# Kernel optimization log

Hardware: AMD Instinct MI355X
Metric: run time of the kernel (lower is better)

## Reference

```python
import jax, jax.numpy as jnp
import numpy as np

MARGIN = 1.0
EPS = 1e-12  # safe sqrt/normalize clamp; used entries have magnitude >> EPS


def _normalize(x):
    return x / jnp.maximum(jnp.linalg.norm(x, axis=-1, keepdims=True), EPS)


def _cdist(x, y):
    # Pairwise L2 distances, matches torch.cdist(p=2)
    sq = (jnp.sum(x * x, axis=-1)[:, None]
          + jnp.sum(y * y, axis=-1)[None, :]
          - 2.0 * (x @ y.T))
    return jnp.sqrt(jnp.maximum(sq, EPS))


def setup_inputs() -> dict:
    key = jax.random.key(0)
    k1, k2, k3 = jax.random.split(key, 3)
    B, P, D = 4096, 2, 256
    anchor = jax.random.normal(k1, (B, D), dtype=jnp.float32)
    positive = jax.random.normal(k2, (B, P, D), dtype=jnp.float32)
    labels = jax.random.randint(k3, (B,), 0, 200)
    return {"anchor": anchor, "positive": positive, "labels": labels}


def reference(anchor, positive, labels):
    a = _normalize(anchor)            # [B, D]
    p = _normalize(positive)          # [B, P, D]
    B = a.shape[0]
    all_labels = jnp.concatenate([labels, labels])           # [2B]
    neg_mask = all_labels[None, :] != labels[:, None]        # [B, 2B]
    idx = jnp.arange(B)
    losses = []
    for v in range(p.shape[1]):  # loop over small fixed num_positives
        feats = jnp.concatenate([a, p[:, v]], axis=0)        # [2B, D]
        dist = _cdist(feats, feats)                          # [2B, 2B]
        pos_dist = dist[idx, idx + B]                        # [B]
        # hard negative mining: min distance over different-label columns
        neg_dist = jnp.min(jnp.where(neg_mask, dist[:B], jnp.inf), axis=1)  # [B]
        losses.append(jnp.maximum(pos_dist - neg_dist + MARGIN, 0.0))
    return jnp.mean(jnp.stack(losses))
```

## Files before the change

### kernel.cpp

```cpp
#include <hip/hip_runtime.h>
#include <hip/hip_bf16.h>

#define NB    4096
#define ND    256
#define NP    2
#define TOT   (NB * 3)
#define NCHUNK 24
#define COLS_PER_CHUNK (TOT / NCHUNK)
#define TILES (COLS_PER_CHUNK / 16)
#define PITCH 528
#define NEG_INIT (-4.0f)

typedef __bf16 bf16x8 __attribute__((ext_vector_type(8)));
typedef float  f32x4  __attribute__((ext_vector_type(4)));

#define WS_F_OFF    0
#define WS_POS_OFF  (TOT * ND * 2)
#define WS_PART_OFF (WS_POS_OFF + NB * NP * 4)

__device__ __forceinline__ unsigned short f2bf(float f) {
    unsigned u = __float_as_uint(f);
    u += 0x7fffu + ((u >> 16) & 1u);
    return (unsigned short)(u >> 16);
}

__global__ void norm_pos_kernel(const float* __restrict__ anchor,
                                const float* __restrict__ positive,
                                unsigned short* __restrict__ F,
                                float* __restrict__ posArr) {
    int wid = threadIdx.x >> 6, lane = threadIdx.x & 63;
    int row = blockIdx.x * 4 + wid;
    if (row < NB) {
        const float* src = anchor + (size_t)row * ND;
        float4 x = *(const float4*)(src + lane * 4);
        float ss = x.x * x.x + x.y * x.y + x.z * x.z + x.w * x.w;
        #pragma unroll
        for (int m = 1; m < 64; m <<= 1) ss += __shfl_xor(ss, m, 64);
        float inv = 1.0f / fmaxf(sqrtf(ss), 1e-12f);
        ushort4 o;
        o.x = f2bf(x.x * inv); o.y = f2bf(x.y * inv);
        o.z = f2bf(x.z * inv); o.w = f2bf(x.w * inv);
        *(ushort4*)(F + (size_t)row * ND + lane * 4) = o;
    } else {
        int q = row - NB;
        int v = q >> 12;
        int j = q & (NB - 1);
        const float* sp = positive + (size_t)(j * NP + v) * ND;
        const float* sa = anchor + (size_t)j * ND;
        float4 xp = *(const float4*)(sp + lane * 4);
        float4 xa = *(const float4*)(sa + lane * 4);
        float sspv = xp.x * xp.x + xp.y * xp.y + xp.z * xp.z + xp.w * xp.w;
        float ssa  = xa.x * xa.x + xa.y * xa.y + xa.z * xa.z + xa.w * xa.w;
        float dot  = xa.x * xp.x + xa.y * xp.y + xa.z * xp.z + xa.w * xp.w;
        #pragma unroll
        for (int m = 1; m < 64; m <<= 1) {
            sspv += __shfl_xor(sspv, m, 64);
            ssa  += __shfl_xor(ssa, m, 64);
            dot  += __shfl_xor(dot, m, 64);
        }
        float invp = 1.0f / fmaxf(sqrtf(sspv), 1e-12f);
        ushort4 o;
        o.x = f2bf(xp.x * invp); o.y = f2bf(xp.y * invp);
        o.z = f2bf(xp.z * invp); o.w = f2bf(xp.w * invp);
        *(ushort4*)(F + (size_t)row * ND + lane * 4) = o;
        if (lane == 0) {
            float inva = 1.0f / fmaxf(sqrtf(ssa), 1e-12f);
            float dn = dot * inva * invp;
            float sq = 2.0f - 2.0f * dn;
            posArr[j * NP + v] = sqrtf(fmaxf(sq, 1e-12f));
        }
    }
}

__global__ __launch_bounds__(256) void gram_max_kernel(
        const unsigned short* __restrict__ F,
        const int* __restrict__ labels,
        float* __restrict__ partials) {
    __shared__ unsigned char lds[2][16 * PITCH];
    int tid = threadIdx.x;
    int wid = tid >> 6, lane = tid & 63;
    int l15 = lane & 15, quad = lane >> 4;
    int rowBase = blockIdx.x * 128 + wid * 32;
    int chunk = blockIdx.y;
    int col0 = chunk * COLS_PER_CHUNK;
    int part = col0 >> 12;
    const unsigned char* Fb = (const unsigned char*)F;

    int scol = tid >> 4, sseg = tid & 15;

    bf16x8 af[2][8];
    #pragma unroll
    for (int s = 0; s < 2; ++s) {
        const unsigned char* ar = Fb + (size_t)(rowBase + s * 16 + l15) * 512 + quad * 16;
        #pragma unroll
        for (int kk = 0; kk < 8; ++kk)
            af[s][kk] = *(const bf16x8*)(ar + kk * 64);
    }
    int rl[2][4];
    #pragma unroll
    for (int s = 0; s < 2; ++s)
        #pragma unroll
        for (int r = 0; r < 4; ++r)
            rl[s][r] = labels[rowBase + s * 16 + quad * 4 + r];

    float vmax[2][4];
    #pragma unroll
    for (int s = 0; s < 2; ++s)
        #pragma unroll
        for (int r = 0; r < 4; ++r) vmax[s][r] = NEG_INIT;

    float4 r0, r1;
    auto gload = [&](int ct) {
        const unsigned char* g = Fb + (size_t)(col0 + ct * 16 + scol) * 512 + sseg * 16;
        r0 = *(const float4*)g;
        r1 = *(const float4*)(g + 256);
    };
    auto swrite = [&](int buf) {
        unsigned char* p = &lds[buf][scol * PITCH + sseg * 16];
        *(float4*)p = r0;
        *(float4*)(p + 256) = r1;
    };

    gload(0); swrite(0);
    gload(1);
    __syncthreads();

    for (int ct = 0; ct < TILES; ++ct) {
        int buf = ct & 1;
        bf16x8 bfr[8];
        #pragma unroll
        for (int kk = 0; kk < 8; ++kk)
            bfr[kk] = *(const bf16x8*)&lds[buf][l15 * PITCH + quad * 16 + kk * 64];

        if (ct + 1 < TILES) swrite(buf ^ 1);
        if (ct + 2 < TILES) gload(ct + 2);

        int c = col0 + ct * 16 + l15;
        int lc = labels[c & (NB - 1)];

        f32x4 acc0a = {0.f,0.f,0.f,0.f}, acc0b = {0.f,0.f,0.f,0.f};
        f32x4 acc1a = {0.f,0.f,0.f,0.f}, acc1b = {0.f,0.f,0.f,0.f};
        #pragma unroll
        for (int kk = 0; kk < 4; ++kk) {
            acc0a = __builtin_amdgcn_mfma_f32_16x16x32_bf16(af[0][kk],   bfr[kk],   acc0a, 0, 0, 0);
            acc0b = __builtin_amdgcn_mfma_f32_16x16x32_bf16(af[0][kk+4], bfr[kk+4], acc0b, 0, 0, 0);
            acc1a = __builtin_amdgcn_mfma_f32_16x16x32_bf16(af[1][kk],   bfr[kk],   acc1a, 0, 0, 0);
            acc1b = __builtin_amdgcn_mfma_f32_16x16x32_bf16(af[1][kk+4], bfr[kk+4], acc1b, 0, 0, 0);
        }
        #pragma unroll
        for (int r = 0; r < 4; ++r) {
            float d0 = acc0a[r] + acc0b[r], d1 = acc1a[r] + acc1b[r];
            vmax[0][r] = fmaxf(vmax[0][r], (lc != rl[0][r]) ? d0 : NEG_INIT);
            vmax[1][r] = fmaxf(vmax[1][r], (lc != rl[1][r]) ? d1 : NEG_INIT);
        }
        __syncthreads();
    }

    #pragma unroll
    for (int m = 1; m < 16; m <<= 1)
        #pragma unroll
        for (int s = 0; s < 2; ++s)
            #pragma unroll
            for (int r = 0; r < 4; ++r)
                vmax[s][r] = fmaxf(vmax[s][r], __shfl_xor(vmax[s][r], m, 64));

    if (l15 == 0) {
        #pragma unroll
        for (int s = 0; s < 2; ++s)
            #pragma unroll
            for (int r = 0; r < 4; ++r) {
                int row = rowBase + s * 16 + quad * 4 + r;
                partials[(size_t)part * NB * 8 + (size_t)row * 8 + (chunk & 7)] = vmax[s][r];
            }
    }
}

__global__ void finalize_kernel(const float* __restrict__ partials,
                                const float* __restrict__ posArr,
                                float* __restrict__ out) {
    int row = blockIdx.x * 256 + threadIdx.x;
    const float* pa = partials + (size_t)row * 8;
    const float* pb = pa + (size_t)NB * 8;
    const float* pc = pb + (size_t)NB * 8;
    float ma = NEG_INIT, m0 = NEG_INIT, m1 = NEG_INIT;
    #pragma unroll
    for (int j = 0; j < 8; ++j) {
        ma = fmaxf(ma, pa[j]);
        m0 = fmaxf(m0, pb[j]);
        m1 = fmaxf(m1, pc[j]);
    }
    float n0 = sqrtf(fmaxf(2.0f - 2.0f * fmaxf(ma, m0), 1e-12f));
    float n1 = sqrtf(fmaxf(2.0f - 2.0f * fmaxf(ma, m1), 1e-12f));
    float l = fmaxf(posArr[row * 2 + 0] - n0 + 1.0f, 0.0f)
            + fmaxf(posArr[row * 2 + 1] - n1 + 1.0f, 0.0f);
    int lane = threadIdx.x & 63, wid = threadIdx.x >> 6;
    #pragma unroll
    for (int m = 1; m < 64; m <<= 1) l += __shfl_xor(l, m, 64);
    __shared__ float wsum[4];
    if (lane == 0) wsum[wid] = l;
    __syncthreads();
    if (threadIdx.x == 0) {
        float s = wsum[0] + wsum[1] + wsum[2] + wsum[3];
        atomicAdd(out, s * (1.0f / (NB * NP)));
    }
}

extern "C" void kernel_launch(void* const* d_in, const int* in_sizes, int n_in,
                              void* d_out, int out_size, void* d_ws, size_t ws_size,
                              hipStream_t stream) {
    const float* anchor   = (const float*)d_in[0];
    const float* positive = (const float*)d_in[1];
    const int*   labels   = (const int*)d_in[2];
    float* out = (float*)d_out;

    unsigned short* F = (unsigned short*)((char*)d_ws + WS_F_OFF);
    float* posArr     = (float*)((char*)d_ws + WS_POS_OFF);
    float* partials   = (float*)((char*)d_ws + WS_PART_OFF);

    norm_pos_kernel<<<TOT / 4, 256, 0, stream>>>(anchor, positive, F, posArr);
    gram_max_kernel<<<dim3(NB / 128, NCHUNK), 256, 0, stream>>>(F, labels, partials);
    hipMemsetAsync(d_out, 0, sizeof(float), stream);
    finalize_kernel<<<NB / 256, 256, 0, stream>>>(partials, posArr, out);
}
```

Before: 102.7 us.

## Give each wave 64 rows, halve block size, stage column labels in LDS

The Gram/max kernel now runs 2 waves per block, each holding 64 A rows (4 MFMA row tiles) instead of 32, so every B tile loaded from LDS feeds twice as many MFMAs. Column labels are preloaded into shared memory once per block, and row labels are packed as bytes so four label comparisons become one XOR. The aim is to raise MFMA work per LDS read and cut per-tile label loads, at the cost of more registers per thread and fewer waves per block, which may lower occupancy and latency hiding. Byte packing assumes labels are below 256.

```diff
diff --git a/kernel.cpp b/kernel.cpp
--- a/kernel.cpp
+++ b/kernel.cpp
@@ -72,53 +72,57 @@
     }
 }
 
-__global__ __launch_bounds__(256) void gram_max_kernel(
+__global__ __launch_bounds__(128) void gram_max_kernel(
         const unsigned short* __restrict__ F,
         const int* __restrict__ labels,
         float* __restrict__ partials) {
     __shared__ unsigned char lds[2][16 * PITCH];
+    __shared__ int slab[COLS_PER_CHUNK];
     int tid = threadIdx.x;
     int wid = tid >> 6, lane = tid & 63;
     int l15 = lane & 15, quad = lane >> 4;
-    int rowBase = blockIdx.x * 128 + wid * 32;
+    int rowBase = blockIdx.x * 128 + wid * 64;
     int chunk = blockIdx.y;
     int col0 = chunk * COLS_PER_CHUNK;
     int part = col0 >> 12;
     const unsigned char* Fb = (const unsigned char*)F;
 
-    int scol = tid >> 4, sseg = tid & 15;
-
-    bf16x8 af[2][8];
-    #pragma unroll
-    for (int s = 0; s < 2; ++s) {
+    ((int4*)slab)[tid] = ((const int4*)(labels + (col0 & (NB - 1))))[tid];
+
+    int scol = tid >> 3, sseg = tid & 7;
+
+    bf16x8 af[4][8];
+    #pragma unroll
+    for (int s = 0; s < 4; ++s) {
         const unsigned char* ar = Fb + (size_t)(rowBase + s * 16 + l15) * 512 + quad * 16;
         #pragma unroll
         for (int kk = 0; kk < 8; ++kk)
             af[s][kk] = *(const bf16x8*)(ar + kk * 64);
     }
-    int rl[2][4];
-    #pragma unroll
-    for (int s = 0; s < 2; ++s)
-        #pragma unroll
-        for (int r = 0; r < 4; ++r)
-            rl[s][r] = labels[rowBase + s * 16 + quad * 4 + r];
-
-    float vmax[2][4];
-    #pragma unroll
-    for (int s = 0; s < 2; ++s)
+    unsigned rlp[4];
+    #pragma unroll
+    for (int s = 0; s < 4; ++s) {
+        const int* lb = labels + rowBase + s * 16 + quad * 4;
+        rlp[s] = (unsigned)lb[0] | ((unsigned)lb[1] << 8)
+               | ((unsigned)lb[2] << 16) | ((unsigned)lb[3] << 24);
+    }
+
+    float vmax[4][4];
+    #pragma unroll
+    for (int s = 0; s < 4; ++s)
         #pragma unroll
         for (int r = 0; r < 4; ++r) vmax[s][r] = NEG_INIT;
 
-    float4 r0, r1;
+    float4 rg[4];
     auto gload = [&](int ct) {
-        const unsigned char* g = Fb + (size_t)(col0 + ct * 16 + scol) * 512 + sseg * 16;
-        r0 = *(const float4*)g;
-        r1 = *(const float4*)(g + 256);
+        const unsigned char* g = Fb + (size_t)(col0 + ct * 16 + scol) * 512 + sseg * 64;
+        #pragma unroll
+        for (int j = 0; j < 4; ++j) rg[j] = *(const float4*)(g + j * 16);
     };
     auto swrite = [&](int buf) {
-        unsigned char* p = &lds[buf][scol * PITCH + sseg * 16];
-        *(float4*)p = r0;
-        *(float4*)(p + 256) = r1;
+        unsigned char* p = &lds[buf][scol * PITCH + sseg * 64];
+        #pragma unroll
+        for (int j = 0; j < 4; ++j) *(float4*)(p + j * 16) = rg[j];
     };
 
     gload(0); swrite(0);
@@ -135,23 +139,26 @@
         if (ct + 1 < TILES) swrite(buf ^ 1);
         if (ct + 2 < TILES) gload(ct + 2);
 
-        int c = col0 + ct * 16 + l15;
-        int lc = labels[c & (NB - 1)];
-
-        f32x4 acc0a = {0.f,0.f,0.f,0.f}, acc0b = {0.f,0.f,0.f,0.f};
-        f32x4 acc1a = {0.f,0.f,0.f,0.f}, acc1b = {0.f,0.f,0.f,0.f};
-        #pragma unroll
-        for (int kk = 0; kk < 4; ++kk) {
-            acc0a = __builtin_amdgcn_mfma_f32_16x16x32_bf16(af[0][kk],   bfr[kk],   acc0a, 0, 0, 0);
-            acc0b = __builtin_amdgcn_mfma_f32_16x16x32_bf16(af[0][kk+4], bfr[kk+4], acc0b, 0, 0, 0);
-            acc1a = __builtin_amdgcn_mfma_f32_16x16x32_bf16(af[1][kk],   bfr[kk],   acc1a, 0, 0, 0);
-            acc1b = __builtin_amdgcn_mfma_f32_16x16x32_bf16(af[1][kk+4], bfr[kk+4], acc1b, 0, 0, 0);
-        }
-        #pragma unroll
-        for (int r = 0; r < 4; ++r) {
-            float d0 = acc0a[r] + acc0b[r], d1 = acc1a[r] + acc1b[r];
-            vmax[0][r] = fmaxf(vmax[0][r], (lc != rl[0][r]) ? d0 : NEG_INIT);
-            vmax[1][r] = fmaxf(vmax[1][r], (lc != rl[1][r]) ? d1 : NEG_INIT);
+        int lc = slab[ct * 16 + l15];
+        unsigned lcq = (unsigned)lc * 0x01010101u;
+
+        f32x4 acc[4];
+        #pragma unroll
+        for (int s = 0; s < 4; ++s) acc[s] = (f32x4){0.f, 0.f, 0.f, 0.f};
+        #pragma unroll
+        for (int kk = 0; kk < 8; ++kk)
+            #pragma unroll
+            for (int s = 0; s < 4; ++s)
+                acc[s] = __builtin_amdgcn_mfma_f32_16x16x32_bf16(af[s][kk], bfr[kk], acc[s], 0, 0, 0);
+
+        #pragma unroll
+        for (int s = 0; s < 4; ++s) {
+            unsigned x = rlp[s] ^ lcq;
+            #pragma unroll
+            for (int r = 0; r < 4; ++r) {
+                bool neq = ((x >> (8 * r)) & 0xffu) != 0u;
+                vmax[s][r] = fmaxf(vmax[s][r], neq ? acc[s][r] : NEG_INIT);
+            }
         }
         __syncthreads();
     }
@@ -159,14 +166,14 @@
     #pragma unroll
     for (int m = 1; m < 16; m <<= 1)
         #pragma unroll
-        for (int s = 0; s < 2; ++s)
+        for (int s = 0; s < 4; ++s)
             #pragma unroll
             for (int r = 0; r < 4; ++r)
                 vmax[s][r] = fmaxf(vmax[s][r], __shfl_xor(vmax[s][r], m, 64));
 
     if (l15 == 0) {
         #pragma unroll
-        for (int s = 0; s < 2; ++s)
+        for (int s = 0; s < 4; ++s)
             #pragma unroll
             for (int r = 0; r < 4; ++r) {
                 int row = rowBase + s * 16 + quad * 4 + r;
@@ -218,7 +225,7 @@
     float* partials   = (float*)((char*)d_ws + WS_PART_OFF);
 
     norm_pos_kernel<<<TOT / 4, 256, 0, stream>>>(anchor, positive, F, posArr);
-    gram_max_kernel<<<dim3(NB / 128, NCHUNK), 256, 0, stream>>>(F, labels, partials);
+    gram_max_kernel<<<dim3(NB / 128, NCHUNK), 128, 0, stream>>>(F, labels, partials);
     hipMemsetAsync(d_out, 0, sizeof(float), stream);
     finalize_kernel<<<NB / 256, 256, 0, stream>>>(partials, posArr, out);
 }
```

New measurement: 129.5 us. +26.0%, slower.
